# Kernel optimization log

Hardware: AMD Instinct MI355X
Metric: run time of the kernel (lower is better)

## Reference

```python
import jax, jax.numpy as jnp
import numpy as np

DIM = 64

def conv2d_g2(x, w, b):
    # 3x3 conv, padding=1, groups=2, NCHW
    y = jax.lax.conv_general_dilated(x, w, (1, 1), [(1, 1), (1, 1)],
                                     dimension_numbers=('NCHW', 'OIHW', 'NCHW'),
                                     feature_group_count=2)
    return y + b[None, :, None, None]

def bilinear_gather(x, py, px):
    # x: [B,C,H,W]; py,px: [B,K,H,W] float sample coords -> [B,K,H,W,C]
    B, C, H, W = x.shape
    y0 = jnp.floor(py); x0 = jnp.floor(px)
    ly = py - y0; lx = px - x0
    hy = 1.0 - ly; hx = 1.0 - lx
    b_idx = jnp.arange(B)[:, None, None, None]
    def gather(yi, xi):
        valid = (yi >= 0) & (yi < H) & (xi >= 0) & (xi < W)
        yc = jnp.clip(yi, 0, H - 1).astype(jnp.int32)
        xc = jnp.clip(xi, 0, W - 1).astype(jnp.int32)
        v = x[b_idx, :, yc, xc]  # [B,K,H,W,C]
        return v * valid[..., None].astype(x.dtype)
    return (gather(y0, x0) * (hy * hx)[..., None]
            + gather(y0, x0 + 1) * (hy * lx)[..., None]
            + gather(y0 + 1, x0) * (ly * hx)[..., None]
            + gather(y0 + 1, x0 + 1) * (ly * lx)[..., None])

def deform_dw(x, offset, w, b, k, pad, dil):
    # depthwise (groups=C, offset_groups=1) deformable conv, stride 1
    B, C, H, W = x.shape
    K = k * k
    off = offset.reshape(B, K, 2, H, W)  # torchvision layout: (dy,dx) per kernel tap
    ky = jnp.repeat(jnp.arange(k), k).astype(x.dtype)   # [K]
    kx = jnp.tile(jnp.arange(k), k).astype(x.dtype)     # [K]
    base_y = jnp.arange(H, dtype=x.dtype)[None, None, :, None] - pad + dil * ky[None, :, None, None]
    base_x = jnp.arange(W, dtype=x.dtype)[None, None, None, :] - pad + dil * kx[None, :, None, None]
    py = base_y + off[:, :, 0]  # [B,K,H,W]
    px = base_x + off[:, :, 1]
    val = bilinear_gather(x, py, px)  # [B,K,H,W,C]
    return jnp.einsum('bkhwc,ck->bchw', val, w.reshape(C, K)) + b[None, :, None, None]

def lsk_forward(x, w_off3, b_off3, w_off2, b_off2, w7, b7, w5, b5):
    B, C, H, W = x.shape
    offset3 = conv2d_g2(x, w_off3, b_off3)            # [B,98,H,W]
    out1 = deform_dw(x, offset3, w7, b7, 7, 9, 3)     # [B,C,H,W]
    offset2 = conv2d_g2(x, w_off2, b_off2)            # [B,50,H,W]
    out2 = deform_dw(out1, offset2, w5, b5, 5, 6, 3)  # [B,C,H,W]
    feats = jnp.stack([out1, out2], axis=1)           # [B,2,C,H,W]
    gap = feats.mean(axis=(3, 4), keepdims=True)      # [B,2,C,1,1]
    attn = jax.nn.softmax(gap, axis=1)
    return jnp.sum(feats * attn, axis=1)              # [B,C,H,W]

def setup_inputs() -> dict:
    key = jax.random.key(0)
    ks = jax.random.split(key, 9)
    B, C, H, W = 4, DIM, 56, 56
    return {
        'x':      jax.random.normal(ks[0], (B, C, H, W), jnp.float32),
        'w_off3': jax.random.normal(ks[1], (98, C // 2, 3, 3), jnp.float32) * 0.05,
        'b_off3': jax.random.normal(ks[2], (98,), jnp.float32) * 0.05,
        'w_off2': jax.random.normal(ks[3], (50, C // 2, 3, 3), jnp.float32) * 0.05,
        'b_off2': jax.random.normal(ks[4], (50,), jnp.float32) * 0.05,
        'w7':     jax.random.normal(ks[5], (C, 1, 7, 7), jnp.float32) * 0.1,
        'b7':     jax.random.normal(ks[6], (C,), jnp.float32) * 0.05,
        'w5':     jax.random.normal(ks[7], (C, 1, 5, 5), jnp.float32) * 0.1,
        'b5':     jax.random.normal(ks[8], (C,), jnp.float32) * 0.05,
    }

def reference(x, w_off3, b_off3, w_off2, b_off2, w7, b7, w5, b5):
    return lsk_forward(x, w_off3, b_off3, w_off2, b_off2, w7, b7, w5, b5)
```

## Files before the change

### kernel.cpp

```cpp
#include <hip/hip_runtime.h>
#include <hip/hip_fp16.h>
#include <math.h>

#define HH 56
#define WW 56
#define CC 64
#define BB 4
#define HWA (HH*WW)

typedef _Float16 half8_t __attribute__((ext_vector_type(8)));
typedef _Float16 h2_t   __attribute__((ext_vector_type(2)));
typedef float f32x4_t __attribute__((ext_vector_type(4)));

#define PROWS 57
#define PSTRB (PROWS*57*64*4)
#define ROWSTRB (57*64*4)

#define NB 784

__device__ __forceinline__ void gbar(int* cnt, int target) {
    __syncthreads();
    if (threadIdx.x == 0 && threadIdx.y == 0) {
        __threadfence();
        __hip_atomic_fetch_add(cnt, 1, __ATOMIC_ACQ_REL, __HIP_MEMORY_SCOPE_AGENT);
        int spins = 0;
        while (__hip_atomic_load(cnt, __ATOMIC_ACQUIRE, __HIP_MEMORY_SCOPE_AGENT) < target) {
            __builtin_amdgcn_s_sleep(1);
            if (++spins > (1 << 24)) break;
        }
        __threadfence();
    }
    __syncthreads();
}


__device__ void prep_row(int u, int tid, float* ld,
                         const float* __restrict__ x,
                         __half2* __restrict__ xp, _Float16* __restrict__ xh) {
    int b = u / 56, y = u % 56;
    for (int i = tid; i < 64*56; i += 256) {
        int c = i / 56, col = i % 56;
        ld[c*57 + col] = x[((size_t)b*CC + c)*HWA + y*WW + col];
    }
    __syncthreads();
    for (int i = tid; i < 57*64; i += 256) {
        int j = i >> 6, c = i & 63;
        float lo = (j > 0)  ? ld[c*57 + j - 1] : 0.f;
        float hi = (j < 56) ? ld[c*57 + j]     : 0.f;
        xp[((size_t)(b*PROWS + y)*57 + j)*CC + c] = __floats2half2_rn(lo, hi);
    }
    _Float16* dst = xh + (((size_t)(b*2)*56 + y)*58)*32;
#pragma unroll
    for (int g = 0; g < 2; ++g) {
        for (int i = tid; i < 1856; i += 256) {
            int col = i >> 5, ic = i & 31;
            float v = (col >= 1 && col <= 56) ? ld[(g*32 + ic)*57 + col - 1] : 0.f;
            dst[(size_t)g*(56*58*32) + i] = (_Float16)v;
        }
    }
}

__device__ void pack_unit(int u, int tid,
                          const float* __restrict__ w3, const float* __restrict__ w2,
                          const float* __restrict__ b3, const float* __restrict__ b2,
                          _Float16* __restrict__ Wp, float* __restrict__ bbp) {
    int i = u*256 + tid;
    if (i < 46080) {
        int j    = i & 7;
        int lane = (i >> 3) & 63;
        int mt   = (i >> 9) % 5;
        int kt   = (i / 2560) % 9;
        int g    = i / 23040;
        int m  = mt*16 + (lane & 15);
        int ic = (lane >> 4)*8 + j;
        int ky = kt/3, kx = kt%3;
        float v = 0.f;
        if (m < 49)      v = w3[((g*49 + m)*32 + ic)*9 + ky*3 + kx];
        else if (m < 74) v = w2[((g*25 + (m-49))*32 + ic)*9 + ky*3 + kx];
        Wp[i] = (_Float16)v;
    } else if (i < 46240) {
        int t = i - 46080; int g = t/80, m = t%80;
        float v = 0.f;
        if (m < 49)      v = b3[g*49 + m];
        else if (m < 74) v = b2[g*25 + (m-49)];
        bbp[t] = v;
    }
}

__device__ void conv_unit(int blk, char* smemraw,
                          const _Float16* __restrict__ xh, const _Float16* __restrict__ Wp,
                          const float* __restrict__ bb,
                          float* __restrict__ off3, float* __restrict__ off2) {
    _Float16 (*tile)[3*18*32] = (_Float16(*)[3*18*32])smemraw;
    int iy = blk % 56;
    int g  = (blk / 56) & 1;
    int b  = blk / 112;
    int wv   = threadIdx.y;
    int lane = threadIdx.x;
    int n0 = wv * 16;

    const uint4* xs4 = (const uint4*)xh;
    uint4* tl4 = (uint4*)&tile[wv][0];
#pragma unroll
    for (int i = 0; i < 4; ++i) {
        int idx4 = i*64 + lane;
        if (idx4 < 216) {
            int ic4 = idx4 & 3;
            int seg = idx4 >> 2;
            int cl = seg % 18, r = seg / 18;
            int y = iy - 1 + r, col = n0 + cl;
            uint4 v = {0u, 0u, 0u, 0u};
            if (y >= 0 && y < 56 && col < 58)
                v = xs4[((((size_t)(b*2+g)*56 + y)*58 + col) << 2) + ic4];
            tl4[idx4] = v;
        }
    }
    __syncthreads();

    int nlo = lane & 15, khi = lane >> 4;
    f32x4_t acc[5];
#pragma unroll
    for (int mt = 0; mt < 5; ++mt) acc[mt] = (f32x4_t){0.f,0.f,0.f,0.f};

    const half8_t* wp8 = (const half8_t*)Wp;
#pragma unroll
    for (int kt = 0; kt < 9; ++kt) {
        int ky = kt/3, kx = kt%3;
        half8_t bfrag = *(const half8_t*)&tile[wv][((ky*18) + nlo + kx)*32 + khi*8];
#pragma unroll
        for (int mt = 0; mt < 5; ++mt) {
            half8_t afrag = wp8[(((size_t)g*9 + kt)*5 + mt)*64 + lane];
            acc[mt] = __builtin_amdgcn_mfma_f32_16x16x32_f16(afrag, bfrag, acc[mt], 0, 0, 0);
        }
    }
    __syncthreads();

    int pixcol = n0 + nlo;
    if (pixcol < 56) {
        int pix = iy*WW + pixcol;
#pragma unroll
        for (int mt = 0; mt < 5; ++mt) {
#pragma unroll
            for (int r = 0; r < 4; ++r) {
                int m = mt*16 + khi*4 + r;
                if (m < 74) {
                    float val = acc[mt][r] + bb[g*80 + m];
                    if (m < 49)
                        off3[((size_t)b*98 + g*49 + m)*HWA + pix] = val;
                    else
                        off2[((size_t)b*50 + g*25 + (m-49))*HWA + pix] = val;
                }
            }
        }
    }
}

template<int K, int KS, int PAD, bool WP>
__device__ void deform_unit(int blk, char* smemraw,
                            const _Float16* __restrict__ xp, const float* __restrict__ off,
                            const float* __restrict__ wg, const float* __restrict__ bias,
                            float* __restrict__ out, float* __restrict__ partial,
                            _Float16* __restrict__ xpo) {
    float* lw = (float*)smemraw;
    float (*loffs)[9] = (float(*)[9])(lw + K*65);
    float (*red)[64]  = (float(*)[64])(lw + K*65 + 2*K*9);
    int tid = threadIdx.x + threadIdx.y*64;
    int xcd = blk & 7;
    int idx = blk >> 3;
    int b   = xcd >> 1;
    int hw0 = (xcd & 1)*(HWA/2) + idx*8;

    for (int i = tid; i < K*64; i += 256) {
        int c = i / K, t = i % K;
        lw[t*65 + c] = wg[i];
    }
    for (int i = tid; i < 4*K; i += 256) {
        int row = i >> 1, half = i & 1;
        float4 v = *(const float4*)&off[((size_t)b*2*K + row)*HWA + hw0 + half*4];
        loffs[row][half*4 + 0] = v.x; loffs[row][half*4 + 1] = v.y;
        loffs[row][half*4 + 2] = v.z; loffs[row][half*4 + 3] = v.w;
    }
    __syncthreads();

    int yp = threadIdx.y;
    int c  = threadIdx.x;

    int mx0 = 0, wz0 = 0, ww0 = 0;
    int mx1 = 0, wz1 = 0, ww1 = 0;
    if (c < K) {
        int t = c;
        int ky = t / KS, kx = t % KS;
#pragma unroll
        for (int s = 0; s < 2; ++s) {
            int p = yp + 4*s;
            int hw = hw0 + p;
            int h = hw / WW, w = hw % WW;
            float py = (float)(h - PAD + 3*ky) + loffs[2*t][p];
            float px = (float)(w - PAD + 3*kx) + loffs[2*t+1][p];
            float y0f = floorf(py), x0f = floorf(px);
            float ly = py - y0f, lx = px - x0f;
            float hy = 1.f - ly, hx = 1.f - lx;
            int y0 = (int)y0f, x0 = (int)x0f;
            int j = x0 + 1;
            bool jv = (j >= 0) && (j <= 56);
            int jc = jv ? j : 0;
            float s0 = ((y0   >= 0) && (y0   < HH) && jv) ? hy : 0.f;
            float s1 = ((y0+1 >= 0) && (y0+1 < HH) && jv) ? ly : 0.f;
            bool use1 = (s0 == 0.f);
            int rbase = use1 ? min(max(y0 + 1, 0), 55) : y0;
            float aw = use1 ? s1 : s0;
            float bw = use1 ? 0.f : s1;
            int mxv = (rbase*57 + jc)*(64*4);
            __half2 wah = __floats2half2_rn(aw*hx, aw*lx);
            __half2 wbh = __floats2half2_rn(bw*hx, bw*lx);
            if (s == 0) { mx0 = mxv; wz0 = *(int*)&wah; ww0 = *(int*)&wbh; }
            else        { mx1 = mxv; wz1 = *(int*)&wah; ww1 = *(int*)&wbh; }
        }
    }

    const char* xb = (const char*)xp + (size_t)b*PSTRB;
    float acc0 = 0.f, acc1 = 0.f;
#pragma unroll 4
    for (int t = 0; t < K; ++t) {
        int m0 = (int)__builtin_amdgcn_readlane(mx0, t);
        int z0 = (int)__builtin_amdgcn_readlane(wz0, t);
        int w0 = (int)__builtin_amdgcn_readlane(ww0, t);
        int m1 = (int)__builtin_amdgcn_readlane(mx1, t);
        int z1 = (int)__builtin_amdgcn_readlane(wz1, t);
        int w1 = (int)__builtin_amdgcn_readlane(ww1, t);
        const h2_t* r0p = (const h2_t*)(xb + m0);
        const h2_t* r1p = (const h2_t*)(xb + m0 + ROWSTRB);
        const h2_t* r2p = (const h2_t*)(xb + m1);
        const h2_t* r3p = (const h2_t*)(xb + m1 + ROWSTRB);
        h2_t r0a = r0p[c];
        h2_t r1a = r1p[c];
        h2_t r0b = r2p[c];
        h2_t r1b = r3p[c];
        float lwv = lw[t*65 + c];
        float v0 = __builtin_amdgcn_fdot2(r0a, *(h2_t*)&z0, 0.f, false);
        v0 = __builtin_amdgcn_fdot2(r1a, *(h2_t*)&w0, v0, false);
        float v1 = __builtin_amdgcn_fdot2(r0b, *(h2_t*)&z1, 0.f, false);
        v1 = __builtin_amdgcn_fdot2(r1b, *(h2_t*)&w1, v1, false);
        acc0 = fmaf(v0, lwv, acc0);
        acc1 = fmaf(v1, lwv, acc1);
    }
    float bs = bias[c];
    float val0 = acc0 + bs;
    float val1 = acc1 + bs;
    int hwA = hw0 + yp, hwB = hw0 + yp + 4;
    out[((size_t)b*HWA + hwA)*CC + c] = val0;
    out[((size_t)b*HWA + hwB)*CC + c] = val1;

    if (WP) {
#pragma unroll
        for (int s = 0; s < 2; ++s) {
            int hw = s ? hwB : hwA;
            float val = s ? val1 : val0;
            int y = hw / WW, w = hw % WW;
            _Float16* base = xpo + ((size_t)(b*PROWS + y)*57)*CC*2;
            _Float16 hv = (_Float16)val;
            base[((w    )*64 + c)*2 + 1] = hv;
            base[((w + 1)*64 + c)*2 + 0] = hv;
            if (w == 0)  base[(c)*2 + 0] = (_Float16)0.f;
            if (w == 55) base[((56)*64 + c)*2 + 1] = (_Float16)0.f;
        }
    }

    red[yp][c] = val0;
    red[yp + 4][c] = val1;
    __syncthreads();
    if (yp == 0) {
        float s = red[0][c] + red[1][c] + red[2][c] + red[3][c]
                + red[4][c] + red[5][c] + red[6][c] + red[7][c];
        partial[((size_t)b*(HWA/8) + (hw0 >> 3))*64 + c] = s;
    }
}

__device__ void gap_unit(int blk, int tid, float* redraw,
                         const float* __restrict__ p1, const float* __restrict__ p2,
                         float* __restrict__ g2) {
    float (*red)[64] = (float(*)[64])redraw;
    int chunk = blk % 14;
    int bf    = blk / 14;
    int b     = bf >> 1;
    const float* p = (bf & 1) ? p2 : p1;
    int c = tid & 63, s = tid >> 6;
    float sum = 0.f;
#pragma unroll
    for (int i = 0; i < 7; ++i) {
        int j = chunk*28 + s + 4*i;
        sum += p[((size_t)b*(HWA/8) + j)*64 + c];
    }
    red[s][c] = sum;
    __syncthreads();
    if (s == 0)
        g2[((size_t)bf*14 + chunk)*64 + c]
            = red[0][c] + red[1][c] + red[2][c] + red[3][c];
}

__device__ void combine16(int blk, int tid, float* smemf,
                          const float* __restrict__ o1, const float* __restrict__ o2,
                          const float* __restrict__ g2, float* __restrict__ out) {
    float* ash = smemf;
    float (*tile)[65] = (float(*)[65])(smemf + 128);
    int b  = blk / 196;
    int t0 = (blk % 196) * 16;

    if (tid < 64) {
        float s1 = 0.f, s2 = 0.f;
#pragma unroll
        for (int k = 0; k < 14; ++k) {
            s1 += g2[((size_t)(b*2+0)*14 + k)*64 + tid];
            s2 += g2[((size_t)(b*2+1)*14 + k)*64 + tid];
        }
        s1 *= (1.f/HWA); s2 *= (1.f/HWA);
        float m  = fmaxf(s1, s2);
        float e1 = expf(s1 - m), e2 = expf(s2 - m);
        float a1 = e1 / (e1 + e2);
        ash[tid]      = a1;
        ash[64 + tid] = 1.f - a1;
    }
    __syncthreads();

    int p  = tid >> 4, c4 = tid & 15;
    size_t idx4 = ((size_t)b*HWA + t0 + p)*16 + c4;
    float4 v1 = ((const float4*)o1)[idx4];
    float4 v2 = ((const float4*)o2)[idx4];
    tile[p][c4*4 + 0] = v1.x*ash[c4*4+0] + v2.x*ash[64+c4*4+0];
    tile[p][c4*4 + 1] = v1.y*ash[c4*4+1] + v2.y*ash[64+c4*4+1];
    tile[p][c4*4 + 2] = v1.z*ash[c4*4+2] + v2.z*ash[64+c4*4+2];
    tile[p][c4*4 + 3] = v1.w*ash[c4*4+3] + v2.w*ash[64+c4*4+3];
    __syncthreads();

    int px = tid & 15, c0 = tid >> 4;
#pragma unroll
    for (int i = 0; i < 4; ++i) {
        int c = c0 + 16*i;
        out[((size_t)b*CC + c)*HWA + t0 + px] = tile[px][c];
    }
}


struct KP {
    const float *x, *w3, *b3, *w2, *b2, *w7, *b7, *w5, *b5;
    float *out;
    float *off3, *off2, *out1, *out2;
    __half2 *xp1; _Float16 *xp2, *xh, *Wp;
    float *part1, *part2, *gpA, *bbp;
    int *cnt;
};

__global__ __launch_bounds__(256, 4)
void k_fused(KP p) {
    __shared__ __align__(16) char smem[18432];
    int blk = blockIdx.x;
    int tid = threadIdx.x + threadIdx.y*64;

    if (blk < BB*56)
        prep_row(blk, tid, (float*)smem, p.x, p.xp1, p.xh);
    else if (blk < BB*56 + 181)
        pack_unit(blk - BB*56, tid, p.w3, p.w2, p.b3, p.b2, p.Wp, p.bbp);
    gbar(p.cnt, 1*NB);

    if (blk < BB*2*56)
        conv_unit(blk, smem, p.xh, p.Wp, p.bbp, p.off3, p.off2);
    gbar(p.cnt, 2*NB);

    deform_unit<49,7,9,true>(blk, smem, (const _Float16*)p.xp1, p.off3, p.w7, p.b7,
                             p.out1, p.part1, p.xp2);
    __syncthreads();
    deform_unit<49,7,9,true>(blk + NB, smem, (const _Float16*)p.xp1, p.off3, p.w7, p.b7,
                             p.out1, p.part1, p.xp2);
    gbar(p.cnt, 3*NB);

    deform_unit<25,5,6,false>(blk, smem, p.xp2, p.off2, p.w5, p.b5,
                              p.out2, p.part2, nullptr);
    __syncthreads();
    deform_unit<25,5,6,false>(blk + NB, smem, p.xp2, p.off2, p.w5, p.b5,
                              p.out2, p.part2, nullptr);
    gbar(p.cnt, 4*NB);

    if (blk < 112)
        gap_unit(blk, tid, (float*)smem, p.part1, p.part2, p.gpA);
    gbar(p.cnt, 5*NB);

    combine16(blk, tid, (float*)smem, p.out1, p.out2, p.gpA, p.out);
}


__global__ __launch_bounds__(256)
void k_prep(const float* __restrict__ x,
            const float* __restrict__ w3, const float* __restrict__ w2,
            const float* __restrict__ b3, const float* __restrict__ b2,
            __half2* __restrict__ xp, _Float16* __restrict__ xh,
            _Float16* __restrict__ Wp, float* __restrict__ bbp) {
    __shared__ __align__(16) char smem[14592];
    int blk = blockIdx.x, tid = threadIdx.x;
    if (blk < BB*56) prep_row(blk, tid, (float*)smem, x, xp, xh);
    else             pack_unit(blk - BB*56, tid, w3, w2, b3, b2, Wp, bbp);
}

__global__ __launch_bounds__(256)
void k_convmfma(const _Float16* __restrict__ xh, const _Float16* __restrict__ Wp,
                const float* __restrict__ bb,
                float* __restrict__ off3, float* __restrict__ off2) {
    __shared__ __align__(16) char smem[13824];
    conv_unit(blockIdx.x, smem, xh, Wp, bb, off3, off2);
}

template<int K, int KS, int PAD, bool WP>
__global__ __launch_bounds__(256)
void k_deform(const _Float16* __restrict__ xp, const float* __restrict__ off,
              const float* __restrict__ wg, const float* __restrict__ bias,
              float* __restrict__ out, float* __restrict__ partial,
              _Float16* __restrict__ xpo) {
    __shared__ __align__(16) char smem[18432];
    deform_unit<K,KS,PAD,WP>(blockIdx.x, smem, xp, off, wg, bias, out, partial, xpo);
}

__global__ void k_gapA(const float* __restrict__ p1, const float* __restrict__ p2,
                       float* __restrict__ g2) {
    __shared__ float red[4][64];
    gap_unit(blockIdx.x, threadIdx.x, &red[0][0], p1, p2, g2);
}

__global__ void k_combine16(const float* __restrict__ o1, const float* __restrict__ o2,
                            const float* __restrict__ g2, float* __restrict__ out) {
    __shared__ float smemf[128 + 16*65];
    combine16(blockIdx.x, threadIdx.x, smemf, o1, o2, g2, out);
}


extern "C" void kernel_launch(void* const* d_in, const int* in_sizes, int n_in,
                              void* d_out, int out_size, void* d_ws, size_t ws_size,
                              hipStream_t stream) {
    const float* x      = (const float*)d_in[0];
    const float* w_off3 = (const float*)d_in[1];
    const float* b_off3 = (const float*)d_in[2];
    const float* w_off2 = (const float*)d_in[3];
    const float* b_off2 = (const float*)d_in[4];
    const float* w7     = (const float*)d_in[5];
    const float* b7     = (const float*)d_in[6];
    const float* w5     = (const float*)d_in[7];
    const float* b5     = (const float*)d_in[8];
    float* out = (float*)d_out;

    const size_t PAIRF = (size_t)BB*PROWS*57*64;
    float* ws    = (float*)d_ws;
    float* off3r = ws;
    float* off2r = off3r + 1229312;
    float* out1  = off2r + 627200;
    float* out2  = out1  + 802816;
    float* xp1f  = out2  + 802816;
    float* xp2f  = xp1f  + PAIRF;
    float* xhf   = xp2f  + PAIRF;
    float* part1 = xhf   + 415744;
    float* part2 = part1 + 100352;
    float* gpA   = part2 + 100352;
    float* wpf   = gpA   + 7168;
    float* bbp   = wpf   + 23040;
    float* cntf  = bbp   + 160;
    __half2*  xp1  = (__half2*)xp1f;
    _Float16* xp2h = (_Float16*)xp2f;
    _Float16* xh   = (_Float16*)xhf;
    _Float16* Wp   = (_Float16*)wpf;
    int* cnt = (int*)cntf;
    size_t need = (size_t)(1229312 + 627200 + 802816*2 + 831744*2 + 415744
                           + 100352*2 + 7168 + 23040 + 160 + 16) * 4;
    if (ws_size < need) return;

    int occ = 0;
    hipError_t qe = hipOccupancyMaxActiveBlocksPerMultiprocessor(&occ, k_fused, 256, 0);
    bool fused_ok = (qe == hipSuccess) && (occ * 256 >= NB);

    if (fused_ok) {
        KP kp;
        kp.x = x; kp.w3 = w_off3; kp.b3 = b_off3; kp.w2 = w_off2; kp.b2 = b_off2;
        kp.w7 = w7; kp.b7 = b7; kp.w5 = w5; kp.b5 = b5;
        kp.out = out;
        kp.off3 = off3r; kp.off2 = off2r; kp.out1 = out1; kp.out2 = out2;
        kp.xp1 = xp1; kp.xp2 = xp2h; kp.xh = xh; kp.Wp = Wp;
        kp.part1 = part1; kp.part2 = part2; kp.gpA = gpA; kp.bbp = bbp;
        kp.cnt = cnt;
        hipMemsetAsync(cnt, 0, 64, stream);
        k_fused<<<NB, dim3(64,4), 0, stream>>>(kp);
    } else {
        k_prep<<<BB*56 + 181, 256, 0, stream>>>(x, w_off3, w_off2, b_off3, b_off2,
                                                xp1, xh, Wp, bbp);
        k_convmfma<<<BB*2*56, dim3(64,4), 0, stream>>>(xh, Wp, bbp, off3r, off2r);
        k_deform<49,7,9,true><<<BB*(HWA/8), dim3(64,4), 0, stream>>>(
            (const _Float16*)xp1, off3r, w7, b7, out1, part1, xp2h);
        k_deform<25,5,6,false><<<BB*(HWA/8), dim3(64,4), 0, stream>>>(
            xp2h, off2r, w5, b5, out2, part2, nullptr);
        k_gapA<<<8*14, 256, 0, stream>>>(part1, part2, gpA);
        k_combine16<<<BB*196, 256, 0, stream>>>(out1, out2, gpA, out);
    }
}
```

Baseline: 144.0 us.

## Make fused persistent kernel grid-stride over units and widen combine tiles

Turns the fused kernel's fixed per-block work assignment into grid-stride loops over each stage, so the grid size can follow occupancy (capped at 784) instead of requiring the full grid to be resident. The combine stage now handles 64 pixels per unit instead of 16, using a larger shared tile and float4 reads of the attention weights. It also unrolls the deform tap loop by 8, drops one syncthreads after the conv MFMA loop, and lengthens the barrier spin sleep. The aim is to reduce stage and launch overhead and improve store coalescing, at the cost of more registers from the deeper unroll and a larger combine tile.

Result: slower. 361.4 us (+151.0%).

```diff
diff --git a/kernel.cpp b/kernel.cpp
--- a/kernel.cpp
+++ b/kernel.cpp
@@ -16,8 +16,6 @@
 #define PSTRB (PROWS*57*64*4)
 #define ROWSTRB (57*64*4)
 
-#define NB 784
-
 __device__ __forceinline__ void gbar(int* cnt, int target) {
     __syncthreads();
     if (threadIdx.x == 0 && threadIdx.y == 0) {
@@ -25,7 +23,7 @@
         __hip_atomic_fetch_add(cnt, 1, __ATOMIC_ACQ_REL, __HIP_MEMORY_SCOPE_AGENT);
         int spins = 0;
         while (__hip_atomic_load(cnt, __ATOMIC_ACQUIRE, __HIP_MEMORY_SCOPE_AGENT) < target) {
-            __builtin_amdgcn_s_sleep(1);
+            __builtin_amdgcn_s_sleep(2);
             if (++spins > (1 << 24)) break;
         }
         __threadfence();
@@ -133,7 +131,6 @@
             acc[mt] = __builtin_amdgcn_mfma_f32_16x16x32_f16(afrag, bfrag, acc[mt], 0, 0, 0);
         }
     }
-    __syncthreads();
 
     int pixcol = n0 + nlo;
     if (pixcol < 56) {
@@ -220,7 +217,7 @@
 
     const char* xb = (const char*)xp + (size_t)b*PSTRB;
     float acc0 = 0.f, acc1 = 0.f;
-#pragma unroll 4
+#pragma unroll 8
     for (int t = 0; t < K; ++t) {
         int m0 = (int)__builtin_amdgcn_readlane(mx0, t);
         int z0 = (int)__builtin_amdgcn_readlane(wz0, t);
@@ -298,45 +295,54 @@
             = red[0][c] + red[1][c] + red[2][c] + red[3][c];
 }
 
-__device__ void combine16(int blk, int tid, float* smemf,
-                          const float* __restrict__ o1, const float* __restrict__ o2,
-                          const float* __restrict__ g2, float* __restrict__ out) {
-    float* ash = smemf;
+__device__ void combine_unit(int blk, int tid, float* smemf,
+                             const float* __restrict__ o1, const float* __restrict__ o2,
+                             const float* __restrict__ g2, float* __restrict__ out) {
+    float* ash0 = smemf;
+    float* ash1 = smemf + 64;
     float (*tile)[65] = (float(*)[65])(smemf + 128);
-    int b  = blk / 196;
-    int t0 = (blk % 196) * 16;
+    int b   = blk / (HWA/64);
+    int t0  = (blk % (HWA/64)) * 64;
 
     if (tid < 64) {
+        int cc = tid;
         float s1 = 0.f, s2 = 0.f;
 #pragma unroll
         for (int k = 0; k < 14; ++k) {
-            s1 += g2[((size_t)(b*2+0)*14 + k)*64 + tid];
-            s2 += g2[((size_t)(b*2+1)*14 + k)*64 + tid];
+            s1 += g2[((size_t)(b*2+0)*14 + k)*64 + cc];
+            s2 += g2[((size_t)(b*2+1)*14 + k)*64 + cc];
         }
         s1 *= (1.f/HWA); s2 *= (1.f/HWA);
         float m  = fmaxf(s1, s2);
         float e1 = expf(s1 - m), e2 = expf(s2 - m);
         float a1 = e1 / (e1 + e2);
-        ash[tid]      = a1;
-        ash[64 + tid] = 1.f - a1;
-    }
-    __syncthreads();
-
-    int p  = tid >> 4, c4 = tid & 15;
-    size_t idx4 = ((size_t)b*HWA + t0 + p)*16 + c4;
-    float4 v1 = ((const float4*)o1)[idx4];
-    float4 v2 = ((const float4*)o2)[idx4];
-    tile[p][c4*4 + 0] = v1.x*ash[c4*4+0] + v2.x*ash[64+c4*4+0];
-    tile[p][c4*4 + 1] = v1.y*ash[c4*4+1] + v2.y*ash[64+c4*4+1];
-    tile[p][c4*4 + 2] = v1.z*ash[c4*4+2] + v2.z*ash[64+c4*4+2];
-    tile[p][c4*4 + 3] = v1.w*ash[c4*4+3] + v2.w*ash[64+c4*4+3];
-    __syncthreads();
-
-    int px = tid & 15, c0 = tid >> 4;
+        ash0[cc] = a1;
+        ash1[cc] = 1.f - a1;
+    }
+    __syncthreads();
+
+    const float4* o14 = (const float4*)o1;
+    const float4* o24 = (const float4*)o2;
 #pragma unroll
     for (int i = 0; i < 4; ++i) {
-        int c = c0 + 16*i;
-        out[((size_t)b*CC + c)*HWA + t0 + px] = tile[px][c];
+        int f = i*256 + tid;
+        int p = f >> 4, c4 = f & 15;
+        size_t idx4 = (((size_t)b*HWA + t0 + p)*CC >> 2) + c4;
+        float4 v1 = o14[idx4];
+        float4 v2 = o24[idx4];
+        float4 a1 = *(const float4*)&ash0[c4*4];
+        float4 a2 = *(const float4*)&ash1[c4*4];
+        tile[p][c4*4 + 0] = v1.x*a1.x + v2.x*a2.x;
+        tile[p][c4*4 + 1] = v1.y*a1.y + v2.y*a2.y;
+        tile[p][c4*4 + 2] = v1.z*a1.z + v2.z*a2.z;
+        tile[p][c4*4 + 3] = v1.w*a1.w + v2.w*a2.w;
+    }
+    __syncthreads();
+    int q = tid >> 6, p2 = tid & 63;
+#pragma unroll
+    for (int i = 0; i < 16; ++i) {
+        int c2 = q + 4*i;
+        out[((size_t)b*CC + c2)*HWA + t0 + p2] = tile[p2][c2];
     }
 }
 
@@ -351,40 +357,48 @@
 };
 
 __global__ __launch_bounds__(256, 4)
-void k_fused(KP p) {
+void k_fused(KP p, int NB) {
     __shared__ __align__(16) char smem[18432];
     int blk = blockIdx.x;
     int tid = threadIdx.x + threadIdx.y*64;
 
-    if (blk < BB*56)
-        prep_row(blk, tid, (float*)smem, p.x, p.xp1, p.xh);
-    else if (blk < BB*56 + 181)
-        pack_unit(blk - BB*56, tid, p.w3, p.w2, p.b3, p.b2, p.Wp, p.bbp);
+    for (int u = blk; u < 405; u += NB) {
+        if (u < BB*56) prep_row(u, tid, (float*)smem, p.x, p.xp1, p.xh);
+        else           pack_unit(u - BB*56, tid, p.w3, p.w2, p.b3, p.b2, p.Wp, p.bbp);
+        __syncthreads();
+    }
     gbar(p.cnt, 1*NB);
 
-    if (blk < BB*2*56)
-        conv_unit(blk, smem, p.xh, p.Wp, p.bbp, p.off3, p.off2);
+    for (int u = blk; u < BB*2*56; u += NB) {
+        conv_unit(u, smem, p.xh, p.Wp, p.bbp, p.off3, p.off2);
+        __syncthreads();
+    }
     gbar(p.cnt, 2*NB);
 
-    deform_unit<49,7,9,true>(blk, smem, (const _Float16*)p.xp1, p.off3, p.w7, p.b7,
-                             p.out1, p.part1, p.xp2);
-    __syncthreads();
-    deform_unit<49,7,9,true>(blk + NB, smem, (const _Float16*)p.xp1, p.off3, p.w7, p.b7,
-                             p.out1, p.part1, p.xp2);
+    for (int u = blk; u < BB*(HWA/8); u += NB) {
+        deform_unit<49,7,9,true>(u, smem, (const _Float16*)p.xp1, p.off3, p.w7, p.b7,
+                                 p.out1, p.part1, p.xp2);
+        __syncthreads();
+    }
     gbar(p.cnt, 3*NB);
 
-    deform_unit<25,5,6,false>(blk, smem, p.xp2, p.off2, p.w5, p.b5,
-                              p.out2, p.part2, nullptr);
-    __syncthreads();
-    deform_unit<25,5,6,false>(blk + NB, smem, p.xp2, p.off2, p.w5, p.b5,
-                              p.out2, p.part2, nullptr);
+    for (int u = blk; u < BB*(HWA/8); u += NB) {
+        deform_unit<25,5,6,false>(u, smem, p.xp2, p.off2, p.w5, p.b5,
+                                  p.out2, p.part2, nullptr);
+        __syncthreads();
+    }
     gbar(p.cnt, 4*NB);
 
-    if (blk < 112)
-        gap_unit(blk, tid, (float*)smem, p.part1, p.part2, p.gpA);
+    for (int u = blk; u < 112; u += NB) {
+        gap_unit(u, tid, (float*)smem, p.part1, p.part2, p.gpA);
+        __syncthreads();
+    }
     gbar(p.cnt, 5*NB);
 
-    combine16(blk, tid, (float*)smem, p.out1, p.out2, p.gpA, p.out);
+    for (int u = blk; u < BB*(HWA/64); u += NB) {
+        combine_unit(u, tid, (float*)smem, p.out1, p.out2, p.gpA, p.out);
+        __syncthreads();
+    }
 }
 
 
@@ -394,9 +408,9 @@
             const float* __restrict__ b3, const float* __restrict__ b2,
             __half2* __restrict__ xp, _Float16* __restrict__ xh,
             _Float16* __restrict__ Wp, float* __restrict__ bbp) {
-    __shared__ __align__(16) char smem[14592];
+    __shared__ __align__(16) float ld[64*57];
     int blk = blockIdx.x, tid = threadIdx.x;
-    if (blk < BB*56) prep_row(blk, tid, (float*)smem, x, xp, xh);
+    if (blk < BB*56) prep_row(blk, tid, ld, x, xp, xh);
     else             pack_unit(blk - BB*56, tid, w3, w2, b3, b2, Wp, bbp);
 }
 
@@ -424,10 +438,10 @@
     gap_unit(blockIdx.x, threadIdx.x, &red[0][0], p1, p2, g2);
 }
 
-__global__ void k_combine16(const float* __restrict__ o1, const float* __restrict__ o2,
-                            const float* __restrict__ g2, float* __restrict__ out) {
-    __shared__ float smemf[128 + 16*65];
-    combine16(blockIdx.x, threadIdx.x, smemf, o1, o2, g2, out);
+__global__ void k_combine(const float* __restrict__ o1, const float* __restrict__ o2,
+                          const float* __restrict__ g2, float* __restrict__ out) {
+    __shared__ __align__(16) float smemf[128 + 64*65];
+    combine_unit(blockIdx.x, threadIdx.x, smemf, o1, o2, g2, out);
 }
 
 
@@ -471,9 +485,13 @@
 
     int occ = 0;
     hipError_t qe = hipOccupancyMaxActiveBlocksPerMultiprocessor(&occ, k_fused, 256, 0);
-    bool fused_ok = (qe == hipSuccess) && (occ * 256 >= NB);
-
-    if (fused_ok) {
+    int NB = 0;
+    if (qe == hipSuccess && occ > 0) {
+        NB = occ * 256;
+        if (NB > 784) NB = 784;
+    }
+
+    if (NB > 0) {
         KP kp;
         kp.x = x; kp.w3 = w_off3; kp.b3 = b_off3; kp.w2 = w_off2; kp.b2 = b_off2;
         kp.w7 = w7; kp.b7 = b7; kp.w5 = w5; kp.b5 = b5;
@@ -483,7 +501,7 @@
         kp.part1 = part1; kp.part2 = part2; kp.gpA = gpA; kp.bbp = bbp;
         kp.cnt = cnt;
         hipMemsetAsync(cnt, 0, 64, stream);
-        k_fused<<<NB, dim3(64,4), 0, stream>>>(kp);
+        k_fused<<<NB, dim3(64,4), 0, stream>>>(kp, NB);
     } else {
         k_prep<<<BB*56 + 181, 256, 0, stream>>>(x, w_off3, w_off2, b_off3, b_off2,
                                                 xp1, xh, Wp, bbp);
@@ -493,6 +511,6 @@
         k_deform<25,5,6,false><<<BB*(HWA/8), dim3(64,4), 0, stream>>>(
             xp2h, off2r, w5, b5, out2, part2, nullptr);
         k_gapA<<<8*14, 256, 0, stream>>>(part1, part2, gpA);
-        k_combine16<<<BB*196, 256, 0, stream>>>(out1, out2, gpA, out);
-    }
-}
+        k_combine<<<BB*(HWA/64), 256, 0, stream>>>(out1, out2, gpA, out);
+    }
+}
```
